# Optimization experiments

Measured on AMD Instinct MI355X. Metric: run time of the kernel, lower is better.

The kernel has to match this reference:

```python
import jax, jax.numpy as jnp
import numpy as np
from jax.scipy.special import digamma, gammaln

B, NQ, NK, DM = 8, 2048, 2048, 64
NEG = -1e9


def setup_inputs() -> dict:
    key = jax.random.key(0)
    ks = jax.random.split(key, 9)
    y = jax.random.normal(ks[0], (B, NQ, DM), dtype=jnp.float32)
    x = jax.random.normal(ks[1], (B, NK, DM), dtype=jnp.float32)
    mask = jnp.ones((B, NQ, NK), dtype=jnp.float32)
    eps = jax.random.normal(ks[2], (B, NQ, NK), dtype=jnp.float32)
    # stacked 3-layer MLP params (all layers are DM x DM since d_q=d_k=d_v=d_m)
    Wq = jax.random.normal(ks[3], (3, DM, DM), dtype=jnp.float32) * 0.1
    bq = jnp.zeros((3, DM), dtype=jnp.float32)
    Wk = jax.random.normal(ks[4], (3, DM, DM), dtype=jnp.float32) * 0.1
    bk = jnp.zeros((3, DM), dtype=jnp.float32)
    Wv = jax.random.normal(ks[5], (3, DM, DM), dtype=jnp.float32) * 0.1
    bv = jnp.zeros((3, DM), dtype=jnp.float32)
    return {"y": y, "x": x, "mask": mask, "eps": eps,
            "Wq": Wq, "bq": bq, "Wk": Wk, "bk": bk, "Wv": Wv, "bv": bv}


def _mlp(h, W, b, last_softplus):
    # 3-layer MLP; softplus after first two layers, optionally after last
    for i in range(3):
        h = h @ W[i] + b[i]
        if i < 2 or last_softplus:
            h = jax.nn.softplus(h)
    return h


def _dirichlet_kld(alpha, mask):
    a0 = (alpha * mask).sum(-1, keepdims=True)
    dg_a = digamma(alpha)
    dg_a0 = digamma(a0)
    kl = (gammaln(a0)
          - (gammaln(alpha) * mask).sum(-1, keepdims=True)
          + (alpha * dg_a * mask).sum(-1, keepdims=True)
          - (alpha * dg_a0 * mask).sum(-1, keepdims=True)
          - ((dg_a - dg_a0) * mask).mean(-1, keepdims=True))
    return jnp.abs(kl)


def reference(y, x, mask, eps, Wq, bq, Wk, bk, Wv, bv):
    q = _mlp(y, Wq, bq, True)          # [B,NQ,DM]
    k = _mlp(x, Wk, bk, True)          # [B,NK,DM]
    va = _mlp(x, Wv, bv, False)        # [B,NK,DM]
    qk = jnp.einsum('bqd,bkd->bqk', q, k)
    alpha = qk + 1.0                   # > 1, safe for log/digamma
    log_alpha = jnp.log(alpha)
    mu = (log_alpha - (log_alpha * mask).mean(-1, keepdims=True)) * mask
    latent = mask.sum(-1, keepdims=True)
    inv_a = 1.0 / alpha
    sigma = ((1.0 - 2.0 / latent) * inv_a
             + (1.0 / latent ** 2) * (inv_a * mask).sum(-1, keepdims=True)) * mask
    kld = _dirichlet_kld(alpha, mask).mean()
    neg = (1.0 - mask) * NEG
    attn = jax.nn.softmax(mu + sigma * eps + neg, axis=-1)
    out = attn @ va                    # [B,NQ,DM]
    return out, attn, va, kld
```

## Files before the change

kernel.cpp:

```cpp
#include <hip/hip_runtime.h>
#include <cstdint>
#include <cstddef>

#define BB 8
#define NQ 2048
#define NK 2048
#define DM 64
#define QT 16
#define TPB 512
#define PST 2056

#define LN2f   0.6931471805599453f
#define LOG2Ef 1.4426950408889634f
#define HL2PIf 0.9189385332046727f

typedef float    f4    __attribute__((ext_vector_type(4)));
typedef short    s16x8 __attribute__((ext_vector_type(8)));
typedef unsigned u32x2 __attribute__((ext_vector_type(2)));
typedef unsigned u32x4 __attribute__((ext_vector_type(4)));

__device__ __forceinline__ float frcp(float x){
  float r = __builtin_amdgcn_rcpf(x);
  return r * (2.0f - x*r);
}
__device__ __forceinline__ float softplus(float v){
  return fmaxf(v, 0.0f) + log1pf(__expf(-fabsf(v)));
}
__device__ __forceinline__ float bflo(unsigned u){ return __uint_as_float(u << 16); }
__device__ __forceinline__ float bfhi(unsigned u){ return __uint_as_float(u & 0xffff0000u); }
__device__ __forceinline__ unsigned short f2bf(float f){
  unsigned u = __float_as_uint(f);
  return (unsigned short)((u + 0x7fffu + ((u >> 16) & 1u)) >> 16);
}
__device__ __forceinline__ unsigned pack_rne(float lo, float hi){
  return (unsigned)f2bf(lo) | ((unsigned)f2bf(hi) << 16);
}
__device__ __forceinline__ unsigned cvtpk(float lo, float hi){
  unsigned r;
  asm("v_cvt_pk_bf16_f32 %0, %1, %2" : "=v"(r) : "v"(lo), "v"(hi));
  return r;
}
__device__ __forceinline__ float red32(float v){
  #pragma unroll
  for (int s = 1; s < 32; s <<= 1) v += __shfl_xor(v, s);
  return v;
}

__global__ __launch_bounds__(256) void mlp3_kernel(
    const float* __restrict__ y, const float* __restrict__ x,
    const float* __restrict__ Wq, const float* __restrict__ bq,
    const float* __restrict__ Wk, const float* __restrict__ bk,
    const float* __restrict__ Wv, const float* __restrict__ bv,
    unsigned short* __restrict__ qo, unsigned short* __restrict__ ko,
    float* __restrict__ vo, unsigned short* __restrict__ vaT){
  const int which = blockIdx.y;
  const float* src = (which == 0) ? y : x;
  const float* W   = (which == 0) ? Wq : (which == 1 ? Wk : Wv);
  const float* bb  = (which == 0) ? bq : (which == 1 ? bk : bv);
  const int row0 = blockIdx.x * 64;
  const int t = threadIdx.x;
  const int lane = t & 63, w = t >> 6, lm = lane & 15, lg = lane >> 4;

  __shared__ unsigned short Xl[64][72];
  __shared__ unsigned short Wt[64][72];
  __shared__ float bl[64];

  #pragma unroll
  for (int p = 0; p < 4; ++p){
    int idx = t + p*256;
    int r = idx >> 4, c4 = idx & 15;
    f4 v = ((const f4*)(src + (size_t)row0*DM))[idx];
    u32x2 o = { pack_rne(v.x, v.y), pack_rne(v.z, v.w) };
    *(u32x2*)&Xl[r][c4*4] = o;
  }

  const int wr = w * 16;
  for (int l = 0; l < 3; ++l){
    __syncthreads();
    #pragma unroll
    for (int p = 0; p < 4; ++p){
      int idx = t + p*256;
      int k = idx >> 4, c4 = idx & 15;
      f4 v = ((const f4*)(W + l*DM*DM))[idx];
      Wt[c4*4+0][k] = f2bf(v.x);
      Wt[c4*4+1][k] = f2bf(v.y);
      Wt[c4*4+2][k] = f2bf(v.z);
      Wt[c4*4+3][k] = f2bf(v.w);
    }
    if (t < 64) bl[t] = bb[l*DM + t];
    __syncthreads();
    const bool sp = (l < 2) || (which != 2);
    s16x8 a0 = *(const s16x8*)&Xl[wr + lm][lg*8];
    s16x8 a1 = *(const s16x8*)&Xl[wr + lm][32 + lg*8];
    f4 outv[4];
    #pragma unroll
    for (int nt = 0; nt < 4; ++nt){
      s16x8 b0 = *(const s16x8*)&Wt[nt*16 + lm][lg*8];
      s16x8 b1 = *(const s16x8*)&Wt[nt*16 + lm][32 + lg*8];
      f4 acc = {0.f, 0.f, 0.f, 0.f};
      acc = __builtin_amdgcn_mfma_f32_16x16x32_bf16(a0, b0, acc, 0, 0, 0);
      acc = __builtin_amdgcn_mfma_f32_16x16x32_bf16(a1, b1, acc, 0, 0, 0);
      const float bc = bl[nt*16 + lm];
      #pragma unroll
      for (int r = 0; r < 4; ++r){
        float vv = acc[r] + bc;
        if (sp) vv = softplus(vv);
        acc[r] = vv;
      }
      outv[nt] = acc;
    }
    #pragma unroll
    for (int nt = 0; nt < 4; ++nt)
      #pragma unroll
      for (int r = 0; r < 4; ++r)
        Xl[wr + lg*4 + r][nt*16 + lm] = f2bf(outv[nt][r]);
  }
  __syncthreads();

  if (which != 2){
    unsigned short* dst = ((which == 0) ? qo : ko) + (size_t)row0*DM;
    #pragma unroll
    for (int p = 0; p < 4; ++p){
      int idx = t + p*256;
      int r = idx >> 4, c4 = idx & 15;
      u32x2 u = *(const u32x2*)&Xl[r][c4*4];
      *(u32x2*)(dst + (size_t)idx*4) = u;
    }
  } else {
    #pragma unroll
    for (int p = 0; p < 4; ++p){
      int idx = t + p*256;
      int r = idx >> 4, c4 = idx & 15;
      u32x2 u = *(const u32x2*)&Xl[r][c4*4];
      f4 v = { bflo(u[0]), bfhi(u[0]), bflo(u[1]), bfhi(u[1]) };
      ((f4*)(vo + (size_t)row0*DM))[idx] = v;
    }
    const int bidx = row0 >> 11, jb = row0 & 2047;
    const int d = t >> 2, rs = t & 3;
    u32x4 o0, o1;
    #pragma unroll
    for (int i = 0; i < 4; ++i)
      o0[i] = (unsigned)Xl[rs*16 + 2*i][d] | ((unsigned)Xl[rs*16 + 2*i + 1][d] << 16);
    #pragma unroll
    for (int i = 0; i < 4; ++i)
      o1[i] = (unsigned)Xl[rs*16 + 8 + 2*i][d] | ((unsigned)Xl[rs*16 + 9 + 2*i][d] << 16);
    unsigned short* dst = vaT + ((size_t)bidx*DM + d)*NK + jb + rs*16;
    *(u32x4*)dst       = o0;
    *(u32x4*)(dst + 8) = o1;
  }
}

__global__ __launch_bounds__(TPB, 4) void bayes_main_kernel(
    const unsigned short* __restrict__ qbf, const unsigned short* __restrict__ kbf,
    const unsigned short* __restrict__ vaT,
    const float* __restrict__ maskg, const float* __restrict__ epsg,
    float* __restrict__ outg, float* __restrict__ attng, float* __restrict__ klws){
  const int b  = blockIdx.x & 7;
  const int qt = blockIdx.x >> 3;
  const int q0 = qt * QT;
  const int t  = threadIdx.x;
  const int lane = t & 63, w = t >> 6;
  const int lm = lane & 15, lg = lane >> 4;

  __shared__ unsigned short Plds[QT][PST];
  __shared__ float pvred[4][QT][16];
  __shared__ float rowinvL[QT], klrow[QT];

  {
    const unsigned short* qrow = qbf + ((size_t)(b*NQ + q0 + lm))*DM + lg*8;
    s16x8 qa0 = *(const s16x8*)qrow;
    s16x8 qa1 = *(const s16x8*)(qrow + 32);
    #pragma unroll 2
    for (int tt = 0; tt < 16; ++tt){
      const int jt = w*16 + tt;
      const unsigned short* krow = kbf + ((size_t)(b*NK + jt*16 + lm))*DM + lg*8;
      s16x8 kb0 = *(const s16x8*)krow;
      s16x8 kb1 = *(const s16x8*)(krow + 32);
      f4 acc = {0.f, 0.f, 0.f, 0.f};
      acc = __builtin_amdgcn_mfma_f32_16x16x32_bf16(qa0, kb0, acc, 0, 0, 0);
      acc = __builtin_amdgcn_mfma_f32_16x16x32_bf16(qa1, kb1, acc, 0, 0, 0);
      unsigned p01 = cvtpk(acc[0] + 1.0f, acc[1] + 1.0f);
      unsigned p23 = cvtpk(acc[2] + 1.0f, acc[3] + 1.0f);
      const int col = jt*16 + lm;
      Plds[lg*4 + 0][col] = (unsigned short)(p01 & 0xffffu);
      Plds[lg*4 + 1][col] = (unsigned short)(p01 >> 16);
      Plds[lg*4 + 2][col] = (unsigned short)(p23 & 0xffffu);
      Plds[lg*4 + 3][col] = (unsigned short)(p23 >> 16);
    }
  }
  __syncthreads();

  const int row = t >> 5, c = t & 31;
  const size_t rowoff = ((size_t)(b*NQ) + q0 + row)*NK;

  float a0 = 0, Sl2 = 0, Sinv = 0, Si2 = 0, lat = 0;
  #pragma unroll
  for (int h = 0; h < 2; ++h){
    f4 pm[8];
    #pragma unroll
    for (int k = 0; k < 8; ++k)
      pm[k] = *(const f4*)(maskg + rowoff + (h*8 + k)*128 + c*4);
    #pragma unroll
    for (int k = 0; k < 8; ++k){
      const int kk = h*8 + k;
      u32x2 sw = *(const u32x2*)&Plds[row][kk*128 + c*4];
      const float av[4] = { bflo(sw[0]), bfhi(sw[0]), bflo(sw[1]), bfhi(sw[1]) };
      #pragma unroll
      for (int c4 = 0; c4 < 4; ++c4){
        float a = av[c4], m = pm[k][c4];
        float inv = __builtin_amdgcn_rcpf(a);
        float l2  = __builtin_amdgcn_logf(a);
        a0   = fmaf(a,       m, a0);
        Sl2  = fmaf(l2,      m, Sl2);
        Sinv = fmaf(inv,     m, Sinv);
        Si2  = fmaf(inv*inv, m, Si2);
        lat += m;
      }
    }
  }
  a0 = red32(a0); Sl2 = red32(Sl2); Sinv = red32(Sinv);
  Si2 = red32(Si2); lat = red32(lat);

  const float Sl = Sl2 * LN2f;
  const float invLT = frcp(lat);
  const float c1 = 1.0f - 2.0f*invLT;
  const float S2 = Sinv*invLT*invLT;
  {
    const float la0 = __builtin_amdgcn_logf(a0) * LN2f;
    const float ra0 = frcp(a0);
    const float ra2 = ra0*ra0;
    const float psiA = la0 - 0.5f*ra0 - ra2*(1.0f/12.0f - ra2*(1.0f/120.0f));
    const float lgA  = fmaf(a0 - 0.5f, la0, -a0) + HL2PIf
                     + ra0*(1.0f/12.0f - ra2*(1.0f/360.0f));
    const float gsum = fmaf(0.5f, Sl, a0) - lat*(0.5f + HL2PIf) - Sinv*(1.0f/6.0f);
    const float Sdg  = Sl - 0.5f*Sinv - Si2*(1.0f/12.0f);
    const float kl   = lgA - psiA*a0 + gsum
                     - (Sdg - psiA*lat)*(1.0f/(float)NK);
    if (c == 0) klrow[row] = fabsf(kl);
  }

  const float c1e = c1 * LOG2Ef, S2e = S2 * LOG2Ef;
  float esum = 0.0f;
  u32x2 e2pk[16];
  #pragma unroll
  for (int hb = 0; hb < 4; ++hb){
    f4 pm[4], pe[4];
    #pragma unroll
    for (int j = 0; j < 4; ++j){
      pm[j] = *(const f4*)(maskg + rowoff + (hb*4 + j)*128 + c*4);
      pe[j] = __builtin_nontemporal_load(
          (const f4*)(epsg + rowoff + (hb*4 + j)*128 + c*4));
    }
    #pragma unroll
    for (int j = 0; j < 4; ++j){
      const int kk = hb*4 + j;
      u32x2 sw = *(const u32x2*)&Plds[row][kk*128 + c*4];
      const float av[4] = { bflo(sw[0]), bfhi(sw[0]), bflo(sw[1]), bfhi(sw[1]) };
      float e2v[4];
      #pragma unroll
      for (int c4 = 0; c4 < 4; ++c4){
        float a = av[c4];
        float inv = __builtin_amdgcn_rcpf(a);
        float zz = fmaf(c1e, inv, S2e) * pe[j][c4];
        float p  = __builtin_amdgcn_exp2f(zz);
        float e2 = a * p * pm[j][c4];
        e2v[c4] = e2;
        esum += e2;
      }
      u32x2 ow = { cvtpk(e2v[0], e2v[1]), cvtpk(e2v[2], e2v[3]) };
      e2pk[kk] = ow;
      *(u32x2*)&Plds[row][kk*128 + c*4] = ow;
    }
  }
  esum = red32(esum);
  const float rinv = frcp(esum);
  if (c == 0) rowinvL[row] = rinv;

  #pragma unroll 4
  for (int kk = 0; kk < 16; ++kk){
    u32x2 ew = e2pk[kk];
    f4 o = { bflo(ew[0])*rinv, bfhi(ew[0])*rinv, bflo(ew[1])*rinv, bfhi(ew[1])*rinv };
    __builtin_nontemporal_store(o, (f4*)(attng + rowoff + kk*128 + c*4));
  }
  __syncthreads();

  if (t == 0){
    float s = 0;
    #pragma unroll
    for (int r = 0; r < QT; ++r) s += klrow[r];
    klws[b*(NQ/QT) + qt] = s;
  }

  const int dt = w & 3, jh = w >> 2;
  f4 oacc = {0.f, 0.f, 0.f, 0.f};
  const unsigned short* vrow = vaT + ((size_t)(b*DM) + dt*16 + lm)*NK + jh*1024 + lg*8;
  const unsigned short* prow = &Plds[lm][jh*1024 + lg*8];
  #pragma unroll 4
  for (int ks = 0; ks < 32; ++ks){
    s16x8 pa = *(const s16x8*)(prow + ks*32);
    s16x8 vb = *(const s16x8*)(vrow + ks*32);
    oacc = __builtin_amdgcn_mfma_f32_16x16x32_bf16(pa, vb, oacc, 0, 0, 0);
  }
  if (w >= 4){
    #pragma unroll
    for (int r = 0; r < 4; ++r) pvred[dt][lg*4 + r][lm] = oacc[r];
  }
  __syncthreads();
  if (w < 4){
    #pragma unroll
    for (int r = 0; r < 4; ++r){
      const int q = lg*4 + r;
      float v = (oacc[r] + pvred[dt][q][lm]) * rowinvL[q];
      outg[((size_t)(b*NQ) + q0 + q)*DM + dt*16 + lm] = v;
    }
  }
}

__global__ __launch_bounds__(256) void kld_reduce_kernel(
    const float* __restrict__ klws, float* __restrict__ dst){
  float s = 0.0f;
  for (int i = threadIdx.x; i < BB*(NQ/QT); i += 256) s += klws[i];
  #pragma unroll
  for (int o = 32; o; o >>= 1) s += __shfl_down(s, o);
  __shared__ float w4[4];
  if ((threadIdx.x & 63) == 0) w4[threadIdx.x >> 6] = s;
  __syncthreads();
  if (threadIdx.x == 0)
    dst[0] = (w4[0] + w4[1] + w4[2] + w4[3]) * (1.0f/((float)BB*(float)NQ));
}

extern "C" void kernel_launch(void* const* d_in, const int* in_sizes, int n_in,
                              void* d_out, int out_size, void* d_ws, size_t ws_size,
                              hipStream_t stream){
  const float* y    = (const float*)d_in[0];
  const float* x    = (const float*)d_in[1];
  const float* mask = (const float*)d_in[2];
  const float* eps  = (const float*)d_in[3];
  const float* Wq   = (const float*)d_in[4];
  const float* bq   = (const float*)d_in[5];
  const float* Wk   = (const float*)d_in[6];
  const float* bk   = (const float*)d_in[7];
  const float* Wv   = (const float*)d_in[8];
  const float* bv   = (const float*)d_in[9];

  float* out  = (float*)d_out;
  float* attn = out  + (size_t)BB*NQ*DM;
  float* va   = attn + (size_t)BB*NQ*NK;
  float* kld  = va   + (size_t)BB*NK*DM;

  char* wsb = (char*)d_ws;
  unsigned short* qbf  = (unsigned short*)wsb;
  unsigned short* kbf  = (unsigned short*)(wsb + (size_t)BB*NQ*DM*2);
  unsigned short* vaT  = (unsigned short*)(wsb + (size_t)BB*NQ*DM*4);
  float*          klws = (float*)(wsb + (size_t)BB*NQ*DM*6);

  dim3 gA((BB*NQ)/64, 3);
  hipLaunchKernelGGL(mlp3_kernel, gA, dim3(256), 0, stream,
                     y, x, Wq, bq, Wk, bk, Wv, bv, qbf, kbf, va, vaT);
  hipLaunchKernelGGL(bayes_main_kernel, dim3(BB*(NQ/QT)), dim3(TPB), 0, stream,
                     qbf, kbf, vaT, mask, eps, out, attn, klws);
  hipLaunchKernelGGL(kld_reduce_kernel, dim3(1), dim3(256), 0, stream, klws, kld);
}
```

Measured before the change: 157.2 us.

## Split fused attention kernel into GEMM, sweep and PV kernels via global workspace

The single fused kernel, which kept alpha/P tiles in LDS, is replaced by three kernels. The first computes alpha=qk+1 in bf16 into a global workspace, the second sweeps each row with one wave (stats, KL, softmax numerator, attn write) and overwrites the workspace with the unnormalised P, and the third does P@V with per-row normalisation. The mask is also read only once per row, with a bitmask reused in the second pass. This removes the large LDS footprint and its occupancy limit, at the cost of an extra 64MB-class bf16 round trip through global memory and more launches.

```diff
diff --git a/kernel.cpp b/kernel.cpp
--- a/kernel.cpp
+++ b/kernel.cpp
@@ -7,8 +7,6 @@
 #define NK 2048
 #define DM 64
 #define QT 16
-#define TPB 512
-#define PST 2056
 
 #define LN2f   0.6931471805599453f
 #define LOG2Ef 1.4426950408889634f
@@ -40,9 +38,9 @@
   asm("v_cvt_pk_bf16_f32 %0, %1, %2" : "=v"(r) : "v"(lo), "v"(hi));
   return r;
 }
-__device__ __forceinline__ float red32(float v){
-  #pragma unroll
-  for (int s = 1; s < 32; s <<= 1) v += __shfl_xor(v, s);
+__device__ __forceinline__ float red64(float v){
+  #pragma unroll
+  for (int s = 1; s < 64; s <<= 1) v += __shfl_xor(v, s);
   return v;
 }
 
@@ -150,64 +148,64 @@
   }
 }
 
-__global__ __launch_bounds__(TPB, 4) void bayes_main_kernel(
+__global__ __launch_bounds__(512) void alpha_gemm_kernel(
     const unsigned short* __restrict__ qbf, const unsigned short* __restrict__ kbf,
-    const unsigned short* __restrict__ vaT,
+    unsigned short* __restrict__ Sws){
+  const int b = blockIdx.x & 7, qt = blockIdx.x >> 3, q0 = qt*QT;
+  const int t = threadIdx.x, lane = t & 63, w = t >> 6;
+  const int lm = lane & 15, lg = lane >> 4;
+  const unsigned short* qrow = qbf + ((size_t)(b*NQ + q0 + lm))*DM + lg*8;
+  s16x8 qb0 = *(const s16x8*)qrow;
+  s16x8 qb1 = *(const s16x8*)(qrow + 32);
+  unsigned short* srow = Sws + ((size_t)(b*NQ) + q0 + lm)*NK;
+  #pragma unroll 2
+  for (int tt = 0; tt < 16; ++tt){
+    const int jt = w*16 + tt;
+    const unsigned short* krow = kbf + ((size_t)(b*NK + jt*16 + lm))*DM + lg*8;
+    s16x8 ka0 = *(const s16x8*)krow;
+    s16x8 ka1 = *(const s16x8*)(krow + 32);
+    f4 acc = {0.f, 0.f, 0.f, 0.f};
+    acc = __builtin_amdgcn_mfma_f32_16x16x32_bf16(ka0, qb0, acc, 0, 0, 0);
+    acc = __builtin_amdgcn_mfma_f32_16x16x32_bf16(ka1, qb1, acc, 0, 0, 0);
+    u32x2 o = { cvtpk(acc[0] + 1.0f, acc[1] + 1.0f),
+                cvtpk(acc[2] + 1.0f, acc[3] + 1.0f) };
+    *(u32x2*)(srow + jt*16 + lg*4) = o;
+  }
+}
+
+__global__ __launch_bounds__(256) void sweep_kernel(
+    unsigned short* __restrict__ Sws,
     const float* __restrict__ maskg, const float* __restrict__ epsg,
-    float* __restrict__ outg, float* __restrict__ attng, float* __restrict__ klws){
-  const int b  = blockIdx.x & 7;
-  const int qt = blockIdx.x >> 3;
-  const int q0 = qt * QT;
-  const int t  = threadIdx.x;
-  const int lane = t & 63, w = t >> 6;
-  const int lm = lane & 15, lg = lane >> 4;
-
-  __shared__ unsigned short Plds[QT][PST];
-  __shared__ float pvred[4][QT][16];
-  __shared__ float rowinvL[QT], klrow[QT];
-
-  {
-    const unsigned short* qrow = qbf + ((size_t)(b*NQ + q0 + lm))*DM + lg*8;
-    s16x8 qa0 = *(const s16x8*)qrow;
-    s16x8 qa1 = *(const s16x8*)(qrow + 32);
-    #pragma unroll 2
-    for (int tt = 0; tt < 16; ++tt){
-      const int jt = w*16 + tt;
-      const unsigned short* krow = kbf + ((size_t)(b*NK + jt*16 + lm))*DM + lg*8;
-      s16x8 kb0 = *(const s16x8*)krow;
-      s16x8 kb1 = *(const s16x8*)(krow + 32);
-      f4 acc = {0.f, 0.f, 0.f, 0.f};
-      acc = __builtin_amdgcn_mfma_f32_16x16x32_bf16(qa0, kb0, acc, 0, 0, 0);
-      acc = __builtin_amdgcn_mfma_f32_16x16x32_bf16(qa1, kb1, acc, 0, 0, 0);
-      unsigned p01 = cvtpk(acc[0] + 1.0f, acc[1] + 1.0f);
-      unsigned p23 = cvtpk(acc[2] + 1.0f, acc[3] + 1.0f);
-      const int col = jt*16 + lm;
-      Plds[lg*4 + 0][col] = (unsigned short)(p01 & 0xffffu);
-      Plds[lg*4 + 1][col] = (unsigned short)(p01 >> 16);
-      Plds[lg*4 + 2][col] = (unsigned short)(p23 & 0xffffu);
-      Plds[lg*4 + 3][col] = (unsigned short)(p23 >> 16);
-    }
-  }
-  __syncthreads();
-
-  const int row = t >> 5, c = t & 31;
-  const size_t rowoff = ((size_t)(b*NQ) + q0 + row)*NK;
+    float* __restrict__ attng, float* __restrict__ rowinvws,
+    float* __restrict__ klws){
+  const int b = blockIdx.x & 7, rt = blockIdx.x >> 3;
+  const int t = threadIdx.x, lane = t & 63, w = t >> 6;
+  const int q = rt*4 + w;
+  const size_t rowoff = ((size_t)(b*NQ) + q)*NK;
+  unsigned short* srow = Sws + rowoff;
+
+  u32x2 apk[8];
+  #pragma unroll
+  for (int k = 0; k < 8; ++k)
+    apk[k] = *(const u32x2*)(srow + k*256 + lane*4);
 
   float a0 = 0, Sl2 = 0, Sinv = 0, Si2 = 0, lat = 0;
+  unsigned mbits = 0;
   #pragma unroll
   for (int h = 0; h < 2; ++h){
-    f4 pm[8];
-    #pragma unroll
-    for (int k = 0; k < 8; ++k)
-      pm[k] = *(const f4*)(maskg + rowoff + (h*8 + k)*128 + c*4);
-    #pragma unroll
-    for (int k = 0; k < 8; ++k){
-      const int kk = h*8 + k;
-      u32x2 sw = *(const u32x2*)&Plds[row][kk*128 + c*4];
+    f4 pm[4];
+    #pragma unroll
+    for (int j = 0; j < 4; ++j)
+      pm[j] = *(const f4*)(maskg + rowoff + (h*4 + j)*256 + lane*4);
+    #pragma unroll
+    for (int j = 0; j < 4; ++j){
+      const int kk = h*4 + j;
+      u32x2 sw = apk[kk];
       const float av[4] = { bflo(sw[0]), bfhi(sw[0]), bflo(sw[1]), bfhi(sw[1]) };
       #pragma unroll
       for (int c4 = 0; c4 < 4; ++c4){
-        float a = av[c4], m = pm[k][c4];
+        float a = av[c4], m = pm[j][c4];
+        if (m != 0.0f) mbits |= 1u << (kk*4 + c4);
         float inv = __builtin_amdgcn_rcpf(a);
         float l2  = __builtin_amdgcn_logf(a);
         a0   = fmaf(a,       m, a0);
@@ -218,8 +216,8 @@
       }
     }
   }
-  a0 = red32(a0); Sl2 = red32(Sl2); Sinv = red32(Sinv);
-  Si2 = red32(Si2); lat = red32(lat);
+  a0 = red64(a0); Sl2 = red64(Sl2); Sinv = red64(Sinv);
+  Si2 = red64(Si2); lat = red64(lat);
 
   const float Sl = Sl2 * LN2f;
   const float invLT = frcp(lat);
@@ -236,90 +234,89 @@
     const float Sdg  = Sl - 0.5f*Sinv - Si2*(1.0f/12.0f);
     const float kl   = lgA - psiA*a0 + gsum
                      - (Sdg - psiA*lat)*(1.0f/(float)NK);
-    if (c == 0) klrow[row] = fabsf(kl);
+    if (lane == 0) klws[b*NQ + q] = fabsf(kl);
   }
 
   const float c1e = c1 * LOG2Ef, S2e = S2 * LOG2Ef;
   float esum = 0.0f;
-  u32x2 e2pk[16];
-  #pragma unroll
-  for (int hb = 0; hb < 4; ++hb){
-    f4 pm[4], pe[4];
+  u32x2 e2pk[8];
+  #pragma unroll
+  for (int h = 0; h < 2; ++h){
+    f4 pe[4];
+    #pragma unroll
+    for (int j = 0; j < 4; ++j)
+      pe[j] = __builtin_nontemporal_load(
+          (const f4*)(epsg + rowoff + (h*4 + j)*256 + lane*4));
     #pragma unroll
     for (int j = 0; j < 4; ++j){
-      pm[j] = *(const f4*)(maskg + rowoff + (hb*4 + j)*128 + c*4);
-      pe[j] = __builtin_nontemporal_load(
-          (const f4*)(epsg + rowoff + (hb*4 + j)*128 + c*4));
-    }
-    #pragma unroll
-    for (int j = 0; j < 4; ++j){
-      const int kk = hb*4 + j;
-      u32x2 sw = *(const u32x2*)&Plds[row][kk*128 + c*4];
+      const int kk = h*4 + j;
+      u32x2 sw = apk[kk];
       const float av[4] = { bflo(sw[0]), bfhi(sw[0]), bflo(sw[1]), bfhi(sw[1]) };
       float e2v[4];
       #pragma unroll
       for (int c4 = 0; c4 < 4; ++c4){
         float a = av[c4];
+        float m = ((mbits >> (kk*4 + c4)) & 1u) ? 1.0f : 0.0f;
         float inv = __builtin_amdgcn_rcpf(a);
         float zz = fmaf(c1e, inv, S2e) * pe[j][c4];
-        float p  = __builtin_amdgcn_exp2f(zz);
-        float e2 = a * p * pm[j][c4];
+        float e2 = a * __builtin_amdgcn_exp2f(zz) * m;
         e2v[c4] = e2;
         esum += e2;
       }
-      u32x2 ow = { cvtpk(e2v[0], e2v[1]), cvtpk(e2v[2], e2v[3]) };
-      e2pk[kk] = ow;
-      *(u32x2*)&Plds[row][kk*128 + c*4] = ow;
-    }
-  }
-  esum = red32(esum);
+      e2pk[kk] = (u32x2){ cvtpk(e2v[0], e2v[1]), cvtpk(e2v[2], e2v[3]) };
+    }
+  }
+  esum = red64(esum);
   const float rinv = frcp(esum);
-  if (c == 0) rowinvL[row] = rinv;
-
-  #pragma unroll 4
-  for (int kk = 0; kk < 16; ++kk){
-    u32x2 ew = e2pk[kk];
+  if (lane == 0) rowinvws[b*NQ + q] = rinv;
+
+  #pragma unroll
+  for (int k = 0; k < 8; ++k){
+    *(u32x2*)(srow + k*256 + lane*4) = e2pk[k];
+    u32x2 ew = e2pk[k];
     f4 o = { bflo(ew[0])*rinv, bfhi(ew[0])*rinv, bflo(ew[1])*rinv, bfhi(ew[1])*rinv };
-    __builtin_nontemporal_store(o, (f4*)(attng + rowoff + kk*128 + c*4));
-  }
-  __syncthreads();
-
-  if (t == 0){
-    float s = 0;
-    #pragma unroll
-    for (int r = 0; r < QT; ++r) s += klrow[r];
-    klws[b*(NQ/QT) + qt] = s;
-  }
-
+    __builtin_nontemporal_store(o, (f4*)(attng + rowoff + k*256 + lane*4));
+  }
+}
+
+__global__ __launch_bounds__(512) void pv_kernel(
+    const unsigned short* __restrict__ Sws, const unsigned short* __restrict__ vaT,
+    const float* __restrict__ rowinvws, float* __restrict__ outg){
+  const int b = blockIdx.x & 7, qt = blockIdx.x >> 3, q0 = qt*QT;
+  const int t = threadIdx.x, lane = t & 63, w = t >> 6;
+  const int lm = lane & 15, lg = lane >> 4;
   const int dt = w & 3, jh = w >> 2;
+
+  __shared__ float pvred[4][16][17];
+
   f4 oacc = {0.f, 0.f, 0.f, 0.f};
-  const unsigned short* vrow = vaT + ((size_t)(b*DM) + dt*16 + lm)*NK + jh*1024 + lg*8;
-  const unsigned short* prow = &Plds[lm][jh*1024 + lg*8];
+  const unsigned short* arow = vaT + ((size_t)(b*DM) + dt*16 + lm)*NK + jh*1024 + lg*8;
+  const unsigned short* brow = Sws + ((size_t)(b*NQ) + q0 + lm)*NK + jh*1024 + lg*8;
   #pragma unroll 4
   for (int ks = 0; ks < 32; ++ks){
-    s16x8 pa = *(const s16x8*)(prow + ks*32);
-    s16x8 vb = *(const s16x8*)(vrow + ks*32);
-    oacc = __builtin_amdgcn_mfma_f32_16x16x32_bf16(pa, vb, oacc, 0, 0, 0);
+    s16x8 va8 = *(const s16x8*)(arow + ks*32);
+    s16x8 pb  = *(const s16x8*)(brow + ks*32);
+    oacc = __builtin_amdgcn_mfma_f32_16x16x32_bf16(va8, pb, oacc, 0, 0, 0);
   }
   if (w >= 4){
     #pragma unroll
-    for (int r = 0; r < 4; ++r) pvred[dt][lg*4 + r][lm] = oacc[r];
+    for (int r = 0; r < 4; ++r) pvred[dt][lm][lg*4 + r] = oacc[r];
   }
   __syncthreads();
   if (w < 4){
-    #pragma unroll
-    for (int r = 0; r < 4; ++r){
-      const int q = lg*4 + r;
-      float v = (oacc[r] + pvred[dt][q][lm]) * rowinvL[q];
-      outg[((size_t)(b*NQ) + q0 + q)*DM + dt*16 + lm] = v;
-    }
+    const float rinv = rowinvws[b*NQ + q0 + lm];
+    f4 o;
+    #pragma unroll
+    for (int r = 0; r < 4; ++r)
+      o[r] = (oacc[r] + pvred[dt][lm][lg*4 + r]) * rinv;
+    *(f4*)(outg + ((size_t)(b*NQ) + q0 + lm)*DM + dt*16 + lg*4) = o;
   }
 }
 
 __global__ __launch_bounds__(256) void kld_reduce_kernel(
     const float* __restrict__ klws, float* __restrict__ dst){
   float s = 0.0f;
-  for (int i = threadIdx.x; i < BB*(NQ/QT); i += 256) s += klws[i];
+  for (int i = threadIdx.x; i < BB*NQ; i += 256) s += klws[i];
   #pragma unroll
   for (int o = 32; o; o >>= 1) s += __shfl_down(s, o);
   __shared__ float w4[4];
@@ -349,15 +346,21 @@
   float* kld  = va   + (size_t)BB*NK*DM;
 
   char* wsb = (char*)d_ws;
-  unsigned short* qbf  = (unsigned short*)wsb;
-  unsigned short* kbf  = (unsigned short*)(wsb + (size_t)BB*NQ*DM*2);
-  unsigned short* vaT  = (unsigned short*)(wsb + (size_t)BB*NQ*DM*4);
-  float*          klws = (float*)(wsb + (size_t)BB*NQ*DM*6);
+  unsigned short* qbf   = (unsigned short*)wsb;
+  unsigned short* kbf   = (unsigned short*)(wsb + (size_t)2*1024*1024);
+  unsigned short* vaT   = (unsigned short*)(wsb + (size_t)4*1024*1024);
+  unsigned short* Sws   = (unsigned short*)(wsb + (size_t)6*1024*1024);
+  float*          rowiw = (float*)(wsb + (size_t)6*1024*1024 + (size_t)BB*NQ*NK*2);
+  float*          klws  = rowiw + BB*NQ;
 
   dim3 gA((BB*NQ)/64, 3);
   hipLaunchKernelGGL(mlp3_kernel, gA, dim3(256), 0, stream,
                      y, x, Wq, bq, Wk, bk, Wv, bv, qbf, kbf, va, vaT);
-  hipLaunchKernelGGL(bayes_main_kernel, dim3(BB*(NQ/QT)), dim3(TPB), 0, stream,
-                     qbf, kbf, vaT, mask, eps, out, attn, klws);
+  hipLaunchKernelGGL(alpha_gemm_kernel, dim3(BB*(NQ/QT)), dim3(512), 0, stream,
+                     qbf, kbf, Sws);
+  hipLaunchKernelGGL(sweep_kernel, dim3(BB*(NQ/4)), dim3(256), 0, stream,
+                     Sws, mask, eps, attn, rowiw, klws);
+  hipLaunchKernelGGL(pv_kernel, dim3(BB*(NQ/QT)), dim3(512), 0, stream,
+                     Sws, vaT, rowiw, out);
   hipLaunchKernelGGL(kld_reduce_kernel, dim3(1), dim3(256), 0, stream, klws, kld);
 }
```

Measured after the change: 231.3 us. 1.47x slower.

## Halve query tile to 8 rows, one wave per row, mask bitpacked

Applied to the files above, without the earlier changes.

Reduces the per-block query tile from 16 to 8 rows, so each wave handles a whole row with 64-lane reductions. LDS per block is halved and the launch bound is raised to 8 blocks per CU to get more occupancy. The second mask read is replaced by a per-lane bitmask of nonzero entries, and the packed exp values are re-read from LDS instead of being held in a 16-entry register array. The MFMA stages still compute 16 rows but discard half, which wastes matrix throughput, and the bitmask treats the mask as binary.

```diff
diff --git a/kernel.cpp b/kernel.cpp
--- a/kernel.cpp
+++ b/kernel.cpp
@@ -6,7 +6,7 @@
 #define NQ 2048
 #define NK 2048
 #define DM 64
-#define QT 16
+#define QT 8
 #define TPB 512
 #define PST 2056
 
@@ -40,9 +40,9 @@
   asm("v_cvt_pk_bf16_f32 %0, %1, %2" : "=v"(r) : "v"(lo), "v"(hi));
   return r;
 }
-__device__ __forceinline__ float red32(float v){
-  #pragma unroll
-  for (int s = 1; s < 32; s <<= 1) v += __shfl_xor(v, s);
+__device__ __forceinline__ float red64(float v){
+  #pragma unroll
+  for (int s = 1; s < 64; s <<= 1) v += __shfl_xor(v, s);
   return v;
 }
 
@@ -150,7 +150,7 @@
   }
 }
 
-__global__ __launch_bounds__(TPB, 4) void bayes_main_kernel(
+__global__ __launch_bounds__(TPB, 8) void bayes_main_kernel(
     const unsigned short* __restrict__ qbf, const unsigned short* __restrict__ kbf,
     const unsigned short* __restrict__ vaT,
     const float* __restrict__ maskg, const float* __restrict__ epsg,
@@ -163,11 +163,11 @@
   const int lm = lane & 15, lg = lane >> 4;
 
   __shared__ unsigned short Plds[QT][PST];
-  __shared__ float pvred[4][QT][16];
+  __shared__ float pvred[4][QT][17];
   __shared__ float rowinvL[QT], klrow[QT];
 
   {
-    const unsigned short* qrow = qbf + ((size_t)(b*NQ + q0 + lm))*DM + lg*8;
+    const unsigned short* qrow = qbf + ((size_t)(b*NQ + q0 + (lm & 7)))*DM + lg*8;
     s16x8 qa0 = *(const s16x8*)qrow;
     s16x8 qa1 = *(const s16x8*)(qrow + 32);
     #pragma unroll 2
@@ -179,35 +179,39 @@
       f4 acc = {0.f, 0.f, 0.f, 0.f};
       acc = __builtin_amdgcn_mfma_f32_16x16x32_bf16(qa0, kb0, acc, 0, 0, 0);
       acc = __builtin_amdgcn_mfma_f32_16x16x32_bf16(qa1, kb1, acc, 0, 0, 0);
-      unsigned p01 = cvtpk(acc[0] + 1.0f, acc[1] + 1.0f);
-      unsigned p23 = cvtpk(acc[2] + 1.0f, acc[3] + 1.0f);
-      const int col = jt*16 + lm;
-      Plds[lg*4 + 0][col] = (unsigned short)(p01 & 0xffffu);
-      Plds[lg*4 + 1][col] = (unsigned short)(p01 >> 16);
-      Plds[lg*4 + 2][col] = (unsigned short)(p23 & 0xffffu);
-      Plds[lg*4 + 3][col] = (unsigned short)(p23 >> 16);
-    }
-  }
-  __syncthreads();
-
-  const int row = t >> 5, c = t & 31;
+      if (lg < 2){
+        unsigned p01 = cvtpk(acc[0] + 1.0f, acc[1] + 1.0f);
+        unsigned p23 = cvtpk(acc[2] + 1.0f, acc[3] + 1.0f);
+        const int col = jt*16 + lm;
+        Plds[lg*4 + 0][col] = (unsigned short)(p01 & 0xffffu);
+        Plds[lg*4 + 1][col] = (unsigned short)(p01 >> 16);
+        Plds[lg*4 + 2][col] = (unsigned short)(p23 & 0xffffu);
+        Plds[lg*4 + 3][col] = (unsigned short)(p23 >> 16);
+      }
+    }
+  }
+  __syncthreads();
+
+  const int row = w;
   const size_t rowoff = ((size_t)(b*NQ) + q0 + row)*NK;
 
   float a0 = 0, Sl2 = 0, Sinv = 0, Si2 = 0, lat = 0;
+  unsigned mbits = 0;
   #pragma unroll
   for (int h = 0; h < 2; ++h){
-    f4 pm[8];
-    #pragma unroll
-    for (int k = 0; k < 8; ++k)
-      pm[k] = *(const f4*)(maskg + rowoff + (h*8 + k)*128 + c*4);
-    #pragma unroll
-    for (int k = 0; k < 8; ++k){
-      const int kk = h*8 + k;
-      u32x2 sw = *(const u32x2*)&Plds[row][kk*128 + c*4];
+    f4 pm[4];
+    #pragma unroll
+    for (int j = 0; j < 4; ++j)
+      pm[j] = *(const f4*)(maskg + rowoff + (h*4 + j)*256 + lane*4);
+    #pragma unroll
+    for (int j = 0; j < 4; ++j){
+      const int kk = h*4 + j;
+      u32x2 sw = *(const u32x2*)&Plds[row][kk*256 + lane*4];
       const float av[4] = { bflo(sw[0]), bfhi(sw[0]), bflo(sw[1]), bfhi(sw[1]) };
       #pragma unroll
       for (int c4 = 0; c4 < 4; ++c4){
-        float a = av[c4], m = pm[k][c4];
+        float a = av[c4], m = pm[j][c4];
+        if (m != 0.0f) mbits |= 1u << (kk*4 + c4);
         float inv = __builtin_amdgcn_rcpf(a);
         float l2  = __builtin_amdgcn_logf(a);
         a0   = fmaf(a,       m, a0);
@@ -218,8 +222,8 @@
       }
     }
   }
-  a0 = red32(a0); Sl2 = red32(Sl2); Sinv = red32(Sinv);
-  Si2 = red32(Si2); lat = red32(lat);
+  a0 = red64(a0); Sl2 = red64(Sl2); Sinv = red64(Sinv);
+  Si2 = red64(Si2); lat = red64(lat);
 
   const float Sl = Sl2 * LN2f;
   const float invLT = frcp(lat);
@@ -236,51 +240,47 @@
     const float Sdg  = Sl - 0.5f*Sinv - Si2*(1.0f/12.0f);
     const float kl   = lgA - psiA*a0 + gsum
                      - (Sdg - psiA*lat)*(1.0f/(float)NK);
-    if (c == 0) klrow[row] = fabsf(kl);
+    if (lane == 0) klrow[row] = fabsf(kl);
   }
 
   const float c1e = c1 * LOG2Ef, S2e = S2 * LOG2Ef;
   float esum = 0.0f;
-  u32x2 e2pk[16];
-  #pragma unroll
-  for (int hb = 0; hb < 4; ++hb){
-    f4 pm[4], pe[4];
+  #pragma unroll
+  for (int h = 0; h < 2; ++h){
+    f4 pe[4];
+    #pragma unroll
+    for (int j = 0; j < 4; ++j)
+      pe[j] = __builtin_nontemporal_load(
+          (const f4*)(epsg + rowoff + (h*4 + j)*256 + lane*4));
     #pragma unroll
     for (int j = 0; j < 4; ++j){
-      pm[j] = *(const f4*)(maskg + rowoff + (hb*4 + j)*128 + c*4);
-      pe[j] = __builtin_nontemporal_load(
-          (const f4*)(epsg + rowoff + (hb*4 + j)*128 + c*4));
-    }
-    #pragma unroll
-    for (int j = 0; j < 4; ++j){
-      const int kk = hb*4 + j;
-      u32x2 sw = *(const u32x2*)&Plds[row][kk*128 + c*4];
+      const int kk = h*4 + j;
+      u32x2 sw = *(const u32x2*)&Plds[row][kk*256 + lane*4];
       const float av[4] = { bflo(sw[0]), bfhi(sw[0]), bflo(sw[1]), bfhi(sw[1]) };
       float e2v[4];
       #pragma unroll
       for (int c4 = 0; c4 < 4; ++c4){
         float a = av[c4];
+        float m = ((mbits >> (kk*4 + c4)) & 1u) ? 1.0f : 0.0f;
         float inv = __builtin_amdgcn_rcpf(a);
         float zz = fmaf(c1e, inv, S2e) * pe[j][c4];
-        float p  = __builtin_amdgcn_exp2f(zz);
-        float e2 = a * p * pm[j][c4];
+        float e2 = a * __builtin_amdgcn_exp2f(zz) * m;
         e2v[c4] = e2;
         esum += e2;
       }
       u32x2 ow = { cvtpk(e2v[0], e2v[1]), cvtpk(e2v[2], e2v[3]) };
-      e2pk[kk] = ow;
-      *(u32x2*)&Plds[row][kk*128 + c*4] = ow;
-    }
-  }
-  esum = red32(esum);
+      *(u32x2*)&Plds[row][kk*256 + lane*4] = ow;
+    }
+  }
+  esum = red64(esum);
   const float rinv = frcp(esum);
-  if (c == 0) rowinvL[row] = rinv;
+  if (lane == 0) rowinvL[row] = rinv;
 
   #pragma unroll 4
-  for (int kk = 0; kk < 16; ++kk){
-    u32x2 ew = e2pk[kk];
+  for (int kk = 0; kk < 8; ++kk){
+    u32x2 ew = *(const u32x2*)&Plds[row][kk*256 + lane*4];
     f4 o = { bflo(ew[0])*rinv, bfhi(ew[0])*rinv, bflo(ew[1])*rinv, bfhi(ew[1])*rinv };
-    __builtin_nontemporal_store(o, (f4*)(attng + rowoff + kk*128 + c*4));
+    __builtin_nontemporal_store(o, (f4*)(attng + rowoff + kk*256 + lane*4));
   }
   __syncthreads();
 
@@ -294,7 +294,7 @@
   const int dt = w & 3, jh = w >> 2;
   f4 oacc = {0.f, 0.f, 0.f, 0.f};
   const unsigned short* vrow = vaT + ((size_t)(b*DM) + dt*16 + lm)*NK + jh*1024 + lg*8;
-  const unsigned short* prow = &Plds[lm][jh*1024 + lg*8];
+  const unsigned short* prow = &Plds[lm & 7][jh*1024 + lg*8];
   #pragma unroll 4
   for (int ks = 0; ks < 32; ++ks){
     s16x8 pa = *(const s16x8*)(prow + ks*32);
@@ -302,11 +302,13 @@
     oacc = __builtin_amdgcn_mfma_f32_16x16x32_bf16(pa, vb, oacc, 0, 0, 0);
   }
   if (w >= 4){
-    #pragma unroll
-    for (int r = 0; r < 4; ++r) pvred[dt][lg*4 + r][lm] = oacc[r];
-  }
-  __syncthreads();
-  if (w < 4){
+    if (lg < 2){
+      #pragma unroll
+      for (int r = 0; r < 4; ++r) pvred[dt][lg*4 + r][lm] = oacc[r];
+    }
+  }
+  __syncthreads();
+  if (w < 4 && lg < 2){
     #pragma unroll
     for (int r = 0; r < 4; ++r){
       const int q = lg*4 + r;
```

After: 206.2 us. 31.1% more time.
